# Optimization experiments

Hardware: AMD Instinct MI355X
Metric: run time of the kernel (lower is better)

## Reference

```python
import jax, jax.numpy as jnp
import numpy as np

B, N, C, G = 32, 1024, 64, 64

def setup_inputs() -> dict:
    key = jax.random.key(0)
    ks = jax.random.split(key, 8)
    return {
        "x": jax.random.normal(ks[0], (B, N, C), dtype=jnp.float32),
        "valid_len": jax.random.randint(ks[1], (B,), 0, N, dtype=jnp.int64) if jax.config.jax_enable_x64 else jax.random.randint(ks[1], (B,), 0, N, dtype=jnp.int32),
        "Wq": jax.random.normal(ks[2], (C, G), dtype=jnp.float32) * 0.1,
        "bq": jax.random.normal(ks[3], (G,), dtype=jnp.float32) * 0.1,
        "Wk": jax.random.normal(ks[4], (C, G), dtype=jnp.float32) * 0.1,
        "bk": jax.random.normal(ks[5], (G,), dtype=jnp.float32) * 0.1,
        "Wv": jax.random.normal(ks[6], (C, G), dtype=jnp.float32) * 0.1,
        "bv": jax.random.normal(ks[7], (G,), dtype=jnp.float32) * 0.1,
    }

def reference(x, valid_len, Wq, bq, Wk, bk, Wv, bv):
    # x: [B, N, C]; valid_len: [B] int (number of valid key positions per batch)
    q = x @ Wq + bq                                   # [B, N, G]
    k = x @ Wk + bk                                   # [B, N, G]
    v = x @ Wv + bv                                   # [B, N, G]
    scores = jnp.einsum('bnd,bmd->bnm', q, k)         # [B, N, N] (no 1/sqrt(d) scale)
    # mask: key positions >= valid_len[b] get -1e6 (matches original's -1000000.0 fill)
    col = jnp.arange(scores.shape[-1])
    mask = col[None, None, :] >= valid_len[:, None, None]
    scores = jnp.where(mask, jnp.float32(-1000000.0), scores)
    attn = jax.nn.softmax(scores, axis=-1)            # [B, N, N]
    return jnp.einsum('bnm,bmd->bnd', attn, v)        # [B, N, G]
```

## Files before the change

kernel.cpp:

```cpp
#include <hip/hip_runtime.h>
#include <stdint.h>


typedef __attribute__((ext_vector_type(4))) float    floatx4;
typedef __attribute__((ext_vector_type(8))) _Float16 halfx8;

static __device__ __forceinline__ unsigned short f2h(float f) {
    union { _Float16 h; unsigned short u; } v; v.h = (_Float16)f;
    return v.u;
}
static __device__ __forceinline__ float h2f(unsigned short u) {
    union { unsigned short u; _Float16 h; } v; v.u = u;
    return (float)v.h;
}

#define MFMA16(a, bb, c) __builtin_amdgcn_mfma_f32_16x16x32_f16((a), (bb), (c), 0, 0, 0)

__global__ __launch_bounds__(256, 2) void proj_kernel(
    const float* __restrict__ x,
    const float* __restrict__ Wq, const float* __restrict__ bq,
    const float* __restrict__ Wk, const float* __restrict__ bk,
    const float* __restrict__ Wv, const float* __restrict__ bv,
    unsigned short* __restrict__ qimg,
    unsigned short* __restrict__ kimg,
    unsigned short* __restrict__ vimg)
{
    __shared__ __align__(16) unsigned short sm[24576];
    const int XH = 0, XL = 4096, WQH = 8192, WQL = 12288, WKH = 16384, WVH = 20480;

    const int tid  = threadIdx.x;
    const int blk  = blockIdx.x;
    const int lane = tid & 63;
    const int w    = tid >> 6;
    const int l15  = lane & 15;
    const int quad = lane >> 4;
    const int rl   = lane >> 2;
    const int c8a  = 2 * (lane & 3);
    const int c8b  = c8a + 1;
    const int sidx_a = rl * 64 + ((c8a ^ (rl & 7)) * 8);
    const int sidx_b = rl * 64 + ((c8b ^ (rl & 7)) * 8);

    {
        const float* xrow = x + (size_t)(blk * 64 + w * 16) * 64;
#pragma unroll
        for (int i = 0; i < 2; ++i) {
            int c8   = (i == 0) ? c8a : c8b;
            int sidx = (i == 0) ? sidx_a : sidx_b;
            const float4* gp = (const float4*)(xrow + rl * 64 + c8 * 8);
            float4 f0 = gp[0], f1 = gp[1];
            float fv[8] = { f0.x, f0.y, f0.z, f0.w, f1.x, f1.y, f1.z, f1.w };
            __align__(16) unsigned short thi[8], tlo[8];
#pragma unroll
            for (int j = 0; j < 8; ++j) {
                unsigned short hi = f2h(fv[j]);
                thi[j] = hi;
                tlo[j] = f2h(fv[j] - h2f(hi));
            }
            *(uint4*)&sm[XH + w * 1024 + sidx] = *(uint4*)thi;
            *(uint4*)&sm[XL + w * 1024 + sidx] = *(uint4*)tlo;
        }
    }
    {
        int g = tid & 63, ci = tid >> 6;
#pragma unroll
        for (int j = 0; j < 16; ++j) {
            int c = ci * 16 + j;
            int idx = g * 64 + (((c >> 3) ^ (g & 7)) * 8) + (c & 7);
            float fq = Wq[c * 64 + g];
            unsigned short qhi = f2h(fq);
            sm[WQH + idx] = qhi;
            sm[WQL + idx] = f2h(fq - h2f(qhi));
            sm[WKH + idx] = f2h(Wk[c * 64 + g]);
            sm[WVH + idx] = f2h(Wv[c * 64 + g]);
        }
    }
    __syncthreads();

    const int fidx0 = l15 * 64 + (((0 + quad) ^ (l15 & 7)) * 8);
    const int fidx1 = l15 * 64 + (((4 + quad) ^ (l15 & 7)) * 8);
    halfx8 ah0 = *(const halfx8*)&sm[XH + w * 1024 + fidx0];
    halfx8 ah1 = *(const halfx8*)&sm[XH + w * 1024 + fidx1];
    halfx8 al0 = *(const halfx8*)&sm[XL + w * 1024 + fidx0];
    halfx8 al1 = *(const halfx8*)&sm[XL + w * 1024 + fidx1];

    floatx4 vacc[4];
#pragma unroll
    for (int gs = 0; gs < 4; ++gs) {
        int brow = gs * 16 + l15;
        int b0 = brow * 64 + (((0 + quad) ^ (brow & 7)) * 8);
        int b1 = brow * 64 + (((4 + quad) ^ (brow & 7)) * 8);
        halfx8 bh0 = *(const halfx8*)&sm[WQH + b0];
        halfx8 bh1 = *(const halfx8*)&sm[WQH + b1];
        halfx8 bl0 = *(const halfx8*)&sm[WQL + b0];
        halfx8 bl1 = *(const halfx8*)&sm[WQL + b1];
        halfx8 wk0 = *(const halfx8*)&sm[WKH + b0];
        halfx8 wk1 = *(const halfx8*)&sm[WKH + b1];
        halfx8 wv0 = *(const halfx8*)&sm[WVH + b0];
        halfx8 wv1 = *(const halfx8*)&sm[WVH + b1];

        float bbq = bq[gs * 16 + l15];
        floatx4 qa = { bbq, bbq, bbq, bbq };
        qa = MFMA16(ah0, bh0, qa);
        qa = MFMA16(ah1, bh1, qa);
        qa = MFMA16(ah0, bl0, qa);
        qa = MFMA16(ah1, bl1, qa);
        qa = MFMA16(al0, bh0, qa);
        qa = MFMA16(al1, bh1, qa);

        float bbk = bk[gs * 16 + l15];
        float bbv = bv[gs * 16 + l15];
        floatx4 ka = { bbk, bbk, bbk, bbk };
        floatx4 va = { bbv, bbv, bbv, bbv };
        ka = MFMA16(ah0, wk0, ka);
        ka = MFMA16(ah1, wk1, ka);
        va = MFMA16(ah0, wv0, va);
        va = MFMA16(ah1, wv1, va);
        vacc[gs] = va;

        int c8 = gs * 2 + (l15 >> 3);
#pragma unroll
        for (int r = 0; r < 4; ++r) {
            int row = w * 16 + quad * 4 + r;
            int idx = row * 64 + ((c8 ^ (row & 7)) * 8) + (l15 & 7);
            sm[XH + idx] = f2h(qa[r]);
            sm[XL + idx] = f2h(ka[r]);
        }
    }
    __syncthreads();
#pragma unroll
    for (int gs = 0; gs < 4; ++gs) {
        int g = gs * 16 + l15;
#pragma unroll
        for (int r = 0; r < 4; ++r) {
            int key = w * 16 + quad * 4 + r;
            sm[WQH + g * 64 + (((key >> 3) ^ (g & 7)) * 8) + (key & 7)] = f2h(vacc[gs][r]);
        }
    }
    __syncthreads();

    {
        const size_t tb = (size_t)blk * 4096;
#pragma unroll
        for (int i = 0; i < 2; ++i) {
            int ci = i * 256 + tid;
            *(uint4*)&qimg[tb + ci * 8] = *(const uint4*)&sm[XH  + ci * 8];
            *(uint4*)&kimg[tb + ci * 8] = *(const uint4*)&sm[XL  + ci * 8];
            *(uint4*)&vimg[tb + ci * 8] = *(const uint4*)&sm[WQH + ci * 8];
        }
    }
}

__global__ __launch_bounds__(256, 2) void attn_kernel(
    const unsigned short* __restrict__ qimg,
    const unsigned short* __restrict__ kimg,
    const unsigned short* __restrict__ vimg,
    const int* __restrict__ valid_len, float* __restrict__ out)
{
    __shared__ __align__(16) unsigned short psmem[4096];
    __shared__ int sched[32];

    const int tid  = threadIdx.x;
    const int blk  = blockIdx.x;
    const int lane = tid & 63;
    const int w    = tid >> 6;
    const int l15  = lane & 15;
    const int quad = lane >> 4;

    if (tid < 32) {
        int vlb = valid_len[tid];
        int ntb = (vlb == 0) ? 16 : ((vlb + 63) >> 6);
        int rank = 0;
        for (int b2 = 0; b2 < 32; ++b2) {
            int vl2 = valid_len[b2];
            int nt2 = (vl2 == 0) ? 16 : ((vl2 + 63) >> 6);
            rank += (nt2 > ntb) || (nt2 == ntb && b2 < tid);
        }
        sched[rank] = tid;
    }
    __syncthreads();

    const int b    = (blk < 256) ? sched[blk >> 4] : sched[31 - ((blk - 256) >> 4)];
    const int qt   = blk & 15;
    const int row0 = b * 1024 + qt * 64;

    const int vl    = valid_len[b];
    const int nt    = (vl == 0) ? 16 : ((vl + 63) >> 6);
    const int fullt = vl >> 6;

    const int arow = w * 16 + l15;
    const unsigned short* qb = qimg + (size_t)(b * 16 + qt) * 4096;
    halfx8 aq0 = *(const halfx8*)&qb[arow * 64 + (((0 + quad) ^ (arow & 7)) * 8)];
    halfx8 aq1 = *(const halfx8*)&qb[arow * 64 + (((4 + quad) ^ (arow & 7)) * 8)];

    int idx0[4], idx1[4];
#pragma unroll
    for (int sub = 0; sub < 4; ++sub) {
        int r = sub * 16 + l15;
        idx0[sub] = r * 64 + (((0 + quad) ^ (r & 7)) * 8);
        idx1[sub] = r * 64 + (((4 + quad) ^ (r & 7)) * 8);
    }

    const unsigned short* kt_base = kimg + (size_t)b * 65536;
    const unsigned short* vt_base = vimg + (size_t)b * 65536;

    float m_r[4]    = { -INFINITY, -INFINITY, -INFINITY, -INFINITY };
    float l_lane[4] = { 0.f, 0.f, 0.f, 0.f };
    floatx4 o[4] = { {0,0,0,0}, {0,0,0,0}, {0,0,0,0}, {0,0,0,0} };

    unsigned short* psw = &psmem[w * 1024];

    halfx8 kf0[4], kf1[4];
#pragma unroll
    for (int sub = 0; sub < 4; ++sub) {
        kf0[sub] = *(const halfx8*)&kt_base[idx0[sub]];
        kf1[sub] = *(const halfx8*)&kt_base[idx1[sub]];
    }

    for (int t = 0; t < nt; ++t) {
        const unsigned short* vt = vt_base + (size_t)t * 4096;
        halfx8 vf0[4], vf1[4];
#pragma unroll
        for (int sub = 0; sub < 4; ++sub) {
            vf0[sub] = *(const halfx8*)&vt[idx0[sub]];
            vf1[sub] = *(const halfx8*)&vt[idx1[sub]];
        }

        floatx4 s[4];
#pragma unroll
        for (int sub = 0; sub < 4; ++sub) {
            floatx4 acc = { 0, 0, 0, 0 };
            acc = MFMA16(aq0, kf0[sub], acc);
            acc = MFMA16(aq1, kf1[sub], acc);
            s[sub] = acc;
        }

        const bool pre = (t + 1) < nt;
        halfx8 nk0[4], nk1[4];
        if (pre) {
            const unsigned short* ktn = kt_base + (size_t)(t + 1) * 4096;
#pragma unroll
            for (int sub = 0; sub < 4; ++sub) {
                nk0[sub] = *(const halfx8*)&ktn[idx0[sub]];
                nk1[sub] = *(const halfx8*)&ktn[idx1[sub]];
            }
        }

        if (t >= fullt) {
#pragma unroll
            for (int sub = 0; sub < 4; ++sub) {
                int key = t * 64 + sub * 16 + l15;
                if (key >= vl) { s[sub][0] = -1e6f; s[sub][1] = -1e6f; s[sub][2] = -1e6f; s[sub][3] = -1e6f; }
            }
        }

        float p[4][4];
        float alpha[4];
#pragma unroll
        for (int r = 0; r < 4; ++r) {
            float mx = fmaxf(fmaxf(s[0][r], s[1][r]), fmaxf(s[2][r], s[3][r]));
#pragma unroll
            for (int off = 1; off < 16; off <<= 1)
                mx = fmaxf(mx, __shfl_xor(mx, off, 64));
            float mnew = fmaxf(m_r[r], mx);
            alpha[r] = __expf(m_r[r] - mnew);
            float psum = 0.f;
#pragma unroll
            for (int sub = 0; sub < 4; ++sub) {
                float pv = __expf(s[sub][r] - mnew);
                p[sub][r] = pv;
                psum += pv;
            }
            l_lane[r] = l_lane[r] * alpha[r] + psum;
            m_r[r] = mnew;
        }
#pragma unroll
        for (int gs = 0; gs < 4; ++gs) {
            o[gs][0] *= alpha[0]; o[gs][1] *= alpha[1];
            o[gs][2] *= alpha[2]; o[gs][3] *= alpha[3];
        }

#pragma unroll
        for (int sub = 0; sub < 4; ++sub) {
            int c8 = sub * 2 + (l15 >> 3);
#pragma unroll
            for (int r = 0; r < 4; ++r) {
                int row = quad * 4 + r;
                psw[row * 64 + ((c8 ^ (row & 7)) * 8) + (l15 & 7)] = f2h(p[sub][r]);
            }
        }
        halfx8 ap0 = *(const halfx8*)&psw[l15 * 64 + (((0 + quad) ^ (l15 & 7)) * 8)];
        halfx8 ap1 = *(const halfx8*)&psw[l15 * 64 + (((4 + quad) ^ (l15 & 7)) * 8)];

#pragma unroll
        for (int gs = 0; gs < 4; ++gs) {
            o[gs] = MFMA16(ap0, vf0[gs], o[gs]);
            o[gs] = MFMA16(ap1, vf1[gs], o[gs]);
        }

        if (pre) {
#pragma unroll
            for (int sub = 0; sub < 4; ++sub) {
                kf0[sub] = nk0[sub];
                kf1[sub] = nk1[sub];
            }
        }
    }

    float l[4];
#pragma unroll
    for (int r = 0; r < 4; ++r) {
        float ss = l_lane[r];
#pragma unroll
        for (int off = 1; off < 16; off <<= 1)
            ss += __shfl_xor(ss, off, 64);
        l[r] = ss;
    }
#pragma unroll
    for (int gs = 0; gs < 4; ++gs) {
#pragma unroll
        for (int r = 0; r < 4; ++r) {
            int row = row0 + w * 16 + quad * 4 + r;
            out[row * 64 + gs * 16 + l15] = o[gs][r] / l[r];
        }
    }
}

__global__ __launch_bounds__(256, 2) void fused_attn_fallback(
    const float* __restrict__ x,
    const float* __restrict__ Wq, const float* __restrict__ bq,
    const float* __restrict__ Wk, const float* __restrict__ bk,
    const float* __restrict__ Wv, const float* __restrict__ bv,
    const int* __restrict__ valid_len, float* __restrict__ out)
{
    __shared__ __align__(16) unsigned short smem[28672];
    __shared__ int sched[32];

    const int Q_OFF = 0, XH_OFF = 4096, KL0_OFF = 8192, KL1_OFF = 12288,
              VS0_OFF = 16384, VS1_OFF = 20480, PS_OFF = 24576;

    const int tid  = threadIdx.x;
    const int blk  = blockIdx.x;
    const int lane = tid & 63;
    const int w    = tid >> 6;
    const int l15  = lane & 15;
    const int quad = lane >> 4;

    if (tid < 32) {
        int vlb = valid_len[tid];
        int ntb = (vlb == 0) ? 16 : ((vlb + 63) >> 6);
        int rank = 0;
        for (int b2 = 0; b2 < 32; ++b2) {
            int vl2 = valid_len[b2];
            int nt2 = (vl2 == 0) ? 16 : ((vl2 + 63) >> 6);
            rank += (nt2 > ntb) || (nt2 == ntb && b2 < tid);
        }
        sched[rank] = tid;
    }
    __syncthreads();

    const int hv   = (blk < 256);
    const int b    = hv ? sched[blk >> 4] : sched[31 - ((blk - 256) >> 4)];
    const int n0   = (blk & 15) * 64;
    const int row0 = b * 1024 + n0;

    const int xsl  = XH_OFF + w * 1024;
    const int fidx0 = l15 * 64 + (((0 + quad) ^ (l15 & 7)) * 8);
    const int fidx1 = l15 * 64 + (((4 + quad) ^ (l15 & 7)) * 8);
    const int rl   = lane >> 2;
    const int c8a  = 2 * (lane & 3);
    const int c8b  = 2 * (lane & 3) + 1;
    const int sidx_a = rl * 64 + ((c8a ^ (rl & 7)) * 8);
    const int sidx_b = rl * 64 + ((c8b ^ (rl & 7)) * 8);

    const int vl    = valid_len[b];
    const int nt    = (vl == 0) ? 16 : ((vl + 63) >> 6);
    const int fullt = vl >> 6;

    {
        const float* xrow = x + (size_t)(row0 + w * 16) * 64;
#pragma unroll
        for (int i = 0; i < 2; ++i) {
            int c8 = (i == 0) ? c8a : c8b;
            int sidx = (i == 0) ? sidx_a : sidx_b;
            const float4* gp = (const float4*)(xrow + rl * 64 + c8 * 8);
            float4 f0 = gp[0], f1 = gp[1];
            float fv[8] = { f0.x, f0.y, f0.z, f0.w, f1.x, f1.y, f1.z, f1.w };
            __align__(16) unsigned short thi[8], tlo[8];
#pragma unroll
            for (int j = 0; j < 8; ++j) {
                unsigned short hi = f2h(fv[j]);
                thi[j] = hi;
                tlo[j] = f2h(fv[j] - h2f(hi));
            }
            *(uint4*)&smem[xsl + sidx]                = *(uint4*)thi;
            *(uint4*)&smem[VS0_OFF + w * 1024 + sidx] = *(uint4*)tlo;
        }
    }
    {
        int g = tid & 63, ci = tid >> 6;
#pragma unroll
        for (int j = 0; j < 16; ++j) {
            int c = ci * 16 + j;
            int idx = g * 64 + (((c >> 3) ^ (g & 7)) * 8) + (c & 7);
            float fq = Wq[c * 64 + g];
            unsigned short qhi = f2h(fq);
            smem[KL0_OFF + idx] = qhi;
            smem[KL1_OFF + idx] = f2h(fq - h2f(qhi));
            smem[VS1_OFF + idx] = f2h(Wk[c * 64 + g]);
            smem[PS_OFF  + idx] = f2h(Wv[c * 64 + g]);
        }
    }
    __syncthreads();

    halfx8 wkf0[4], wkf1[4], wvf0[4], wvf1[4];
#pragma unroll
    for (int gs = 0; gs < 4; ++gs) {
        int brow = gs * 16 + l15;
        int b0 = brow * 64 + (((0 + quad) ^ (brow & 7)) * 8);
        int b1 = brow * 64 + (((4 + quad) ^ (brow & 7)) * 8);
        wkf0[gs] = *(const halfx8*)&smem[VS1_OFF + b0];
        wkf1[gs] = *(const halfx8*)&smem[VS1_OFF + b1];
        wvf0[gs] = *(const halfx8*)&smem[PS_OFF + b0];
        wvf1[gs] = *(const halfx8*)&smem[PS_OFF + b1];
    }

    {
        halfx8 ah0 = *(const halfx8*)&smem[xsl + fidx0];
        halfx8 ah1 = *(const halfx8*)&smem[xsl + fidx1];
        halfx8 al0 = *(const halfx8*)&smem[VS0_OFF + w * 1024 + fidx0];
        halfx8 al1 = *(const halfx8*)&smem[VS0_OFF + w * 1024 + fidx1];
#pragma unroll
        for (int gs = 0; gs < 4; ++gs) {
            int brow = gs * 16 + l15;
            float bb = bq[gs * 16 + l15];
            floatx4 acc = { bb, bb, bb, bb };
            int b0 = brow * 64 + (((0 + quad) ^ (brow & 7)) * 8);
            int b1 = brow * 64 + (((4 + quad) ^ (brow & 7)) * 8);
            halfx8 bh0 = *(const halfx8*)&smem[KL0_OFF + b0];
            halfx8 bh1 = *(const halfx8*)&smem[KL0_OFF + b1];
            halfx8 bl0 = *(const halfx8*)&smem[KL1_OFF + b0];
            halfx8 bl1 = *(const halfx8*)&smem[KL1_OFF + b1];
            acc = MFMA16(ah0, bh0, acc);
            acc = MFMA16(ah1, bh1, acc);
            acc = MFMA16(ah0, bl0, acc);
            acc = MFMA16(ah1, bl1, acc);
            acc = MFMA16(al0, bh0, acc);
            acc = MFMA16(al1, bh1, acc);
            int c8 = gs * 2 + (l15 >> 3);
#pragma unroll
            for (int r = 0; r < 4; ++r) {
                int row = w * 16 + quad * 4 + r;
                smem[Q_OFF + row * 64 + ((c8 ^ (row & 7)) * 8) + (l15 & 7)] = f2h(acc[r]);
            }
        }
    }
    const int arow = w * 16 + l15;
    halfx8 aq0 = *(const halfx8*)&smem[Q_OFF + arow * 64 + (((0 + quad) ^ (arow & 7)) * 8)];
    halfx8 aq1 = *(const halfx8*)&smem[Q_OFF + arow * 64 + (((4 + quad) ^ (arow & 7)) * 8)];

    {
        const float* xrow = x + (size_t)(b * 1024 + w * 16) * 64;
#pragma unroll
        for (int i = 0; i < 2; ++i) {
            int c8 = (i == 0) ? c8a : c8b;
            int sidx = (i == 0) ? sidx_a : sidx_b;
            const float4* gp = (const float4*)(xrow + rl * 64 + c8 * 8);
            float4 f0 = gp[0], f1 = gp[1];
            __align__(16) unsigned short thi[8] = {
                f2h(f0.x), f2h(f0.y), f2h(f0.z), f2h(f0.w),
                f2h(f1.x), f2h(f1.y), f2h(f1.z), f2h(f1.w) };
            *(uint4*)&smem[xsl + sidx] = *(uint4*)thi;
        }
    }
    __syncthreads();

    {
        halfx8 kxh0 = *(const halfx8*)&smem[xsl + fidx0];
        halfx8 kxh1 = *(const halfx8*)&smem[xsl + fidx1];
#pragma unroll
        for (int gs = 0; gs < 4; ++gs) {
            float bbk = bk[gs * 16 + l15];
            float bbv = bv[gs * 16 + l15];
            floatx4 kacc = { bbk, bbk, bbk, bbk };
            floatx4 vacc = { bbv, bbv, bbv, bbv };
            kacc = MFMA16(kxh0, wkf0[gs], kacc);
            kacc = MFMA16(kxh1, wkf1[gs], kacc);
            vacc = MFMA16(kxh0, wvf0[gs], vacc);
            vacc = MFMA16(kxh1, wvf1[gs], vacc);
            int c8 = gs * 2 + (l15 >> 3);
            int g  = gs * 16 + l15;
#pragma unroll
            for (int r = 0; r < 4; ++r) {
                int key = w * 16 + quad * 4 + r;
                smem[KL0_OFF + key * 64 + ((c8 ^ (key & 7)) * 8) + (l15 & 7)] = f2h(kacc[r]);
                smem[VS0_OFF + g * 64 + (((key >> 3) ^ (g & 7)) * 8) + (key & 7)] = f2h(vacc[r]);
            }
        }
    }

    float m_r[4]    = { -INFINITY, -INFINITY, -INFINITY, -INFINITY };
    float l_lane[4] = { 0.f, 0.f, 0.f, 0.f };
    floatx4 o[4] = { {0,0,0,0}, {0,0,0,0}, {0,0,0,0}, {0,0,0,0} };

    for (int t = 0; t < nt; ++t) {
        bool pre = (t + 1) < nt;
        float4 pfa0, pfa1, pfb0, pfb1;
        if (pre) {
            const float* xrow = x + (size_t)(b * 1024 + (t + 1) * 64 + w * 16) * 64;
            pfa0 = ((const float4*)(xrow + rl * 64 + c8a * 8))[0];
            pfa1 = ((const float4*)(xrow + rl * 64 + c8a * 8))[1];
            pfb0 = ((const float4*)(xrow + rl * 64 + c8b * 8))[0];
            pfb1 = ((const float4*)(xrow + rl * 64 + c8b * 8))[1];
        }
        __syncthreads();

        if (pre) {
            __align__(16) unsigned short ta[8] = {
                f2h(pfa0.x), f2h(pfa0.y), f2h(pfa0.z), f2h(pfa0.w),
                f2h(pfa1.x), f2h(pfa1.y), f2h(pfa1.z), f2h(pfa1.w) };
            __align__(16) unsigned short tb[8] = {
                f2h(pfb0.x), f2h(pfb0.y), f2h(pfb0.z), f2h(pfb0.w),
                f2h(pfb1.x), f2h(pfb1.y), f2h(pfb1.z), f2h(pfb1.w) };
            *(uint4*)&smem[xsl + sidx_a] = *(uint4*)ta;
            *(uint4*)&smem[xsl + sidx_b] = *(uint4*)tb;
            halfx8 kxh0 = *(const halfx8*)&smem[xsl + fidx0];
            halfx8 kxh1 = *(const halfx8*)&smem[xsl + fidx1];
            const int KLn = ((t + 1) & 1) ? KL1_OFF : KL0_OFF;
            const int VSn = ((t + 1) & 1) ? VS1_OFF : VS0_OFF;
#pragma unroll
            for (int gs = 0; gs < 4; ++gs) {
                float bbk = bk[gs * 16 + l15];
                float bbv = bv[gs * 16 + l15];
                floatx4 kacc = { bbk, bbk, bbk, bbk };
                floatx4 vacc = { bbv, bbv, bbv, bbv };
                kacc = MFMA16(kxh0, wkf0[gs], kacc);
                kacc = MFMA16(kxh1, wkf1[gs], kacc);
                vacc = MFMA16(kxh0, wvf0[gs], vacc);
                vacc = MFMA16(kxh1, wvf1[gs], vacc);
                int c8 = gs * 2 + (l15 >> 3);
                int g  = gs * 16 + l15;
#pragma unroll
                for (int r = 0; r < 4; ++r) {
                    int key = w * 16 + quad * 4 + r;
                    smem[KLn + key * 64 + ((c8 ^ (key & 7)) * 8) + (l15 & 7)] = f2h(kacc[r]);
                    smem[VSn + g * 64 + (((key >> 3) ^ (g & 7)) * 8) + (key & 7)] = f2h(vacc[r]);
                }
            }
        }

        const int KLc = (t & 1) ? KL1_OFF : KL0_OFF;
        const int VSc = (t & 1) ? VS1_OFF : VS0_OFF;

        floatx4 s[4];
#pragma unroll
        for (int sub = 0; sub < 4; ++sub) {
            int krow = sub * 16 + l15;
            halfx8 bk0 = *(const halfx8*)&smem[KLc + krow * 64 + (((0 + quad) ^ (krow & 7)) * 8)];
            halfx8 bk1 = *(const halfx8*)&smem[KLc + krow * 64 + (((4 + quad) ^ (krow & 7)) * 8)];
            floatx4 acc = { 0, 0, 0, 0 };
            acc = MFMA16(aq0, bk0, acc);
            acc = MFMA16(aq1, bk1, acc);
            s[sub] = acc;
        }
        if (t >= fullt) {
#pragma unroll
            for (int sub = 0; sub < 4; ++sub) {
                int key = t * 64 + sub * 16 + l15;
                if (key >= vl) { s[sub][0] = -1e6f; s[sub][1] = -1e6f; s[sub][2] = -1e6f; s[sub][3] = -1e6f; }
            }
        }

        float p[4][4];
        float alpha[4];
#pragma unroll
        for (int r = 0; r < 4; ++r) {
            float mx = fmaxf(fmaxf(s[0][r], s[1][r]), fmaxf(s[2][r], s[3][r]));
#pragma unroll
            for (int off = 1; off < 16; off <<= 1)
                mx = fmaxf(mx, __shfl_xor(mx, off, 64));
            float mnew = fmaxf(m_r[r], mx);
            alpha[r] = __expf(m_r[r] - mnew);
            float psum = 0.f;
#pragma unroll
            for (int sub = 0; sub < 4; ++sub) {
                float pv = __expf(s[sub][r] - mnew);
                p[sub][r] = pv;
                psum += pv;
            }
            l_lane[r] = l_lane[r] * alpha[r] + psum;
            m_r[r] = mnew;
        }
#pragma unroll
        for (int gs = 0; gs < 4; ++gs) {
            o[gs][0] *= alpha[0]; o[gs][1] *= alpha[1];
            o[gs][2] *= alpha[2]; o[gs][3] *= alpha[3];
        }

        unsigned short* psw = &smem[PS_OFF + w * 1024];
#pragma unroll
        for (int sub = 0; sub < 4; ++sub) {
            int c8 = sub * 2 + (l15 >> 3);
#pragma unroll
            for (int r = 0; r < 4; ++r) {
                int row = quad * 4 + r;
                psw[row * 64 + ((c8 ^ (row & 7)) * 8) + (l15 & 7)] = f2h(p[sub][r]);
            }
        }
        halfx8 ap0 = *(const halfx8*)&psw[fidx0];
        halfx8 ap1 = *(const halfx8*)&psw[fidx1];

#pragma unroll
        for (int gs = 0; gs < 4; ++gs) {
            int grow = gs * 16 + l15;
            halfx8 bv0 = *(const halfx8*)&smem[VSc + grow * 64 + (((0 + quad) ^ (grow & 7)) * 8)];
            halfx8 bv1 = *(const halfx8*)&smem[VSc + grow * 64 + (((4 + quad) ^ (grow & 7)) * 8)];
            o[gs] = MFMA16(ap0, bv0, o[gs]);
            o[gs] = MFMA16(ap1, bv1, o[gs]);
        }
    }

    float l[4];
#pragma unroll
    for (int r = 0; r < 4; ++r) {
        float ss = l_lane[r];
#pragma unroll
        for (int off = 1; off < 16; off <<= 1)
            ss += __shfl_xor(ss, off, 64);
        l[r] = ss;
    }
#pragma unroll
    for (int gs = 0; gs < 4; ++gs) {
#pragma unroll
        for (int r = 0; r < 4; ++r) {
            int row = row0 + w * 16 + quad * 4 + r;
            out[row * 64 + gs * 16 + l15] = o[gs][r] / l[r];
        }
    }
}

extern "C" void kernel_launch(void* const* d_in, const int* in_sizes, int n_in,
                              void* d_out, int out_size, void* d_ws, size_t ws_size,
                              hipStream_t stream) {
    const float* x    = (const float*)d_in[0];
    const int*   vlen = (const int*)  d_in[1];
    const float* Wq   = (const float*)d_in[2];
    const float* bq   = (const float*)d_in[3];
    const float* Wk   = (const float*)d_in[4];
    const float* bk   = (const float*)d_in[5];
    const float* Wv   = (const float*)d_in[6];
    const float* bv   = (const float*)d_in[7];
    float* out = (float*)d_out;

    const size_t IMG_SHORTS = (size_t)32 * 16 * 4096;
    const size_t NEED = 3 * IMG_SHORTS * sizeof(unsigned short);

    if (ws_size >= NEED) {
        unsigned short* qimg = (unsigned short*)d_ws;
        unsigned short* kimg = qimg + IMG_SHORTS;
        unsigned short* vimg = kimg + IMG_SHORTS;
        proj_kernel<<<512, 256, 0, stream>>>(x, Wq, bq, Wk, bk, Wv, bv,
                                             qimg, kimg, vimg);
        attn_kernel<<<512, 256, 0, stream>>>(qimg, kimg, vimg, vlen, out);
    } else {
        fused_attn_fallback<<<512, 256, 0, stream>>>(
            x, Wq, bq, Wk, bk, Wv, bv, vlen, out);
    }
}
```

Baseline: 99.11 us.

## Process two 64-key tiles per attention loop iteration with K and V register prefetch

```diff
diff --git a/kernel.cpp b/kernel.cpp
--- a/kernel.cpp
+++ b/kernel.cpp
@@ -156,7 +156,7 @@
     const unsigned short* __restrict__ vimg,
     const int* __restrict__ valid_len, float* __restrict__ out)
 {
-    __shared__ __align__(16) unsigned short psmem[4096];
+    __shared__ __align__(16) unsigned short psmem[8192];
     __shared__ int sched[32];
 
     const int tid  = threadIdx.x;
@@ -183,9 +183,9 @@
     const int qt   = blk & 15;
     const int row0 = b * 1024 + qt * 64;
 
-    const int vl    = valid_len[b];
-    const int nt    = (vl == 0) ? 16 : ((vl + 63) >> 6);
-    const int fullt = vl >> 6;
+    const int vl = valid_len[b];
+    const int nt = (vl == 0) ? 16 : ((vl + 63) >> 6);
+    const int np = (nt + 1) >> 1;
 
     const int arow = w * 16 + l15;
     const unsigned short* qb = qimg + (size_t)(b * 16 + qt) * 4096;
@@ -194,11 +194,13 @@
 
     int idx0[4], idx1[4];
 #pragma unroll
-    for (int sub = 0; sub < 4; ++sub) {
-        int r = sub * 16 + l15;
-        idx0[sub] = r * 64 + (((0 + quad) ^ (r & 7)) * 8);
-        idx1[sub] = r * 64 + (((4 + quad) ^ (r & 7)) * 8);
-    }
+    for (int s4 = 0; s4 < 4; ++s4) {
+        int r = s4 * 16 + l15;
+        idx0[s4] = r * 64 + (((0 + quad) ^ (r & 7)) * 8);
+        idx1[s4] = r * 64 + (((4 + quad) ^ (r & 7)) * 8);
+    }
+    const int fp0 = l15 * 64 + (((0 + quad) ^ (l15 & 7)) * 8);
+    const int fp1 = l15 * 64 + (((4 + quad) ^ (l15 & 7)) * 8);
 
     const unsigned short* kt_base = kimg + (size_t)b * 65536;
     const unsigned short* vt_base = vimg + (size_t)b * 65536;
@@ -207,68 +209,72 @@
     float l_lane[4] = { 0.f, 0.f, 0.f, 0.f };
     floatx4 o[4] = { {0,0,0,0}, {0,0,0,0}, {0,0,0,0}, {0,0,0,0} };
 
-    unsigned short* psw = &psmem[w * 1024];
-
-    halfx8 kf0[4], kf1[4];
-#pragma unroll
-    for (int sub = 0; sub < 4; ++sub) {
-        kf0[sub] = *(const halfx8*)&kt_base[idx0[sub]];
-        kf1[sub] = *(const halfx8*)&kt_base[idx1[sub]];
-    }
-
-    for (int t = 0; t < nt; ++t) {
-        const unsigned short* vt = vt_base + (size_t)t * 4096;
-        halfx8 vf0[4], vf1[4];
-#pragma unroll
-        for (int sub = 0; sub < 4; ++sub) {
-            vf0[sub] = *(const halfx8*)&vt[idx0[sub]];
-            vf1[sub] = *(const halfx8*)&vt[idx1[sub]];
-        }
-
-        floatx4 s[4];
-#pragma unroll
-        for (int sub = 0; sub < 4; ++sub) {
+    unsigned short* psw = &psmem[w * 2048];
+
+    halfx8 kf0[8], kf1[8], vf0[8], vf1[8];
+#pragma unroll
+    for (int h = 0; h < 2; ++h) {
+        const unsigned short* kt = kt_base + (size_t)h * 4096;
+        const unsigned short* vt = vt_base + (size_t)h * 4096;
+#pragma unroll
+        for (int s4 = 0; s4 < 4; ++s4) {
+            kf0[h * 4 + s4] = *(const halfx8*)&kt[idx0[s4]];
+            kf1[h * 4 + s4] = *(const halfx8*)&kt[idx1[s4]];
+            vf0[h * 4 + s4] = *(const halfx8*)&vt[idx0[s4]];
+            vf1[h * 4 + s4] = *(const halfx8*)&vt[idx1[s4]];
+        }
+    }
+
+    for (int it = 0; it < np; ++it) {
+        floatx4 s[8];
+#pragma unroll
+        for (int j = 0; j < 8; ++j) {
             floatx4 acc = { 0, 0, 0, 0 };
-            acc = MFMA16(aq0, kf0[sub], acc);
-            acc = MFMA16(aq1, kf1[sub], acc);
-            s[sub] = acc;
-        }
-
-        const bool pre = (t + 1) < nt;
-        halfx8 nk0[4], nk1[4];
+            acc = MFMA16(aq0, kf0[j], acc);
+            acc = MFMA16(aq1, kf1[j], acc);
+            s[j] = acc;
+        }
+
+        const bool pre = (it + 1) < np;
         if (pre) {
-            const unsigned short* ktn = kt_base + (size_t)(t + 1) * 4096;
-#pragma unroll
-            for (int sub = 0; sub < 4; ++sub) {
-                nk0[sub] = *(const halfx8*)&ktn[idx0[sub]];
-                nk1[sub] = *(const halfx8*)&ktn[idx1[sub]];
-            }
-        }
-
-        if (t >= fullt) {
-#pragma unroll
-            for (int sub = 0; sub < 4; ++sub) {
-                int key = t * 64 + sub * 16 + l15;
-                if (key >= vl) { s[sub][0] = -1e6f; s[sub][1] = -1e6f; s[sub][2] = -1e6f; s[sub][3] = -1e6f; }
-            }
-        }
-
-        float p[4][4];
+#pragma unroll
+            for (int h = 0; h < 2; ++h) {
+                const unsigned short* kt = kt_base + (size_t)(2 * (it + 1) + h) * 4096;
+#pragma unroll
+                for (int s4 = 0; s4 < 4; ++s4) {
+                    kf0[h * 4 + s4] = *(const halfx8*)&kt[idx0[s4]];
+                    kf1[h * 4 + s4] = *(const halfx8*)&kt[idx1[s4]];
+                }
+            }
+        }
+
+        if (it * 128 + 128 > vl) {
+#pragma unroll
+            for (int j = 0; j < 8; ++j) {
+                int key = it * 128 + (j >> 2) * 64 + (j & 3) * 16 + l15;
+                if (key >= vl) { s[j][0] = -1e6f; s[j][1] = -1e6f; s[j][2] = -1e6f; s[j][3] = -1e6f; }
+            }
+        }
+
         float alpha[4];
 #pragma unroll
         for (int r = 0; r < 4; ++r) {
-            float mx = fmaxf(fmaxf(s[0][r], s[1][r]), fmaxf(s[2][r], s[3][r]));
+            float mx = fmaxf(fmaxf(fmaxf(s[0][r], s[1][r]), fmaxf(s[2][r], s[3][r])),
+                             fmaxf(fmaxf(s[4][r], s[5][r]), fmaxf(s[6][r], s[7][r])));
 #pragma unroll
             for (int off = 1; off < 16; off <<= 1)
                 mx = fmaxf(mx, __shfl_xor(mx, off, 64));
             float mnew = fmaxf(m_r[r], mx);
             alpha[r] = __expf(m_r[r] - mnew);
             float psum = 0.f;
-#pragma unroll
-            for (int sub = 0; sub < 4; ++sub) {
-                float pv = __expf(s[sub][r] - mnew);
-                p[sub][r] = pv;
+            int row = quad * 4 + r;
+#pragma unroll
+            for (int j = 0; j < 8; ++j) {
+                float pv = __expf(s[j][r] - mnew);
                 psum += pv;
+                int h  = j >> 2;
+                int c8 = (j & 3) * 2 + (l15 >> 3);
+                psw[h * 1024 + row * 64 + ((c8 ^ (row & 7)) * 8) + (l15 & 7)] = f2h(pv);
             }
             l_lane[r] = l_lane[r] * alpha[r] + psum;
             m_r[r] = mnew;
@@ -280,28 +286,25 @@
         }
 
 #pragma unroll
-        for (int sub = 0; sub < 4; ++sub) {
-            int c8 = sub * 2 + (l15 >> 3);
-#pragma unroll
-            for (int r = 0; r < 4; ++r) {
-                int row = quad * 4 + r;
-                psw[row * 64 + ((c8 ^ (row & 7)) * 8) + (l15 & 7)] = f2h(p[sub][r]);
-            }
-        }
-        halfx8 ap0 = *(const halfx8*)&psw[l15 * 64 + (((0 + quad) ^ (l15 & 7)) * 8)];
-        halfx8 ap1 = *(const halfx8*)&psw[l15 * 64 + (((4 + quad) ^ (l15 & 7)) * 8)];
-
-#pragma unroll
-        for (int gs = 0; gs < 4; ++gs) {
-            o[gs] = MFMA16(ap0, vf0[gs], o[gs]);
-            o[gs] = MFMA16(ap1, vf1[gs], o[gs]);
+        for (int h = 0; h < 2; ++h) {
+            halfx8 ap0 = *(const halfx8*)&psw[h * 1024 + fp0];
+            halfx8 ap1 = *(const halfx8*)&psw[h * 1024 + fp1];
+#pragma unroll
+            for (int gs = 0; gs < 4; ++gs) {
+                o[gs] = MFMA16(ap0, vf0[h * 4 + gs], o[gs]);
+                o[gs] = MFMA16(ap1, vf1[h * 4 + gs], o[gs]);
+            }
         }
 
         if (pre) {
 #pragma unroll
-            for (int sub = 0; sub < 4; ++sub) {
-                kf0[sub] = nk0[sub];
-                kf1[sub] = nk1[sub];
+            for (int h = 0; h < 2; ++h) {
+                const unsigned short* vt = vt_base + (size_t)(2 * (it + 1) + h) * 4096;
+#pragma unroll
+                for (int s4 = 0; s4 < 4; ++s4) {
+                    vf0[h * 4 + s4] = *(const halfx8*)&vt[idx0[s4]];
+                    vf1[h * 4 + s4] = *(const halfx8*)&vt[idx1[s4]];
+                }
             }
         }
     }
```

After: 101.6 us. +2.5%, slower.
